# Performance work log

Hardware: AMD Instinct MI355X
Metric: run time of the kernel (lower is better)

The kernel has to match this reference:

```python
import jax, jax.numpy as jnp
import numpy as np

N_HEAD = 16

def setup_inputs() -> dict:
    key = jax.random.key(0)
    k1, k2, k3 = jax.random.split(key, 3)
    B, S, D = 4, 2048, 1024
    x = jax.random.normal(k1, (B, S, D), dtype=jnp.float32)
    w_attn = jax.random.normal(k2, (D, 3 * D), dtype=jnp.float32) * 0.02
    b_attn = jnp.zeros((3 * D,), dtype=jnp.float32)
    w_proj = jax.random.normal(k3, (D, D), dtype=jnp.float32) * 0.02
    b_proj = jnp.zeros((D,), dtype=jnp.float32)
    return {"x": x, "w_attn": w_attn, "b_attn": b_attn, "w_proj": w_proj, "b_proj": b_proj}

def reference(x, w_attn, b_attn, w_proj, b_proj):
    B, S, D = x.shape
    H = N_HEAD
    dh = D // H
    # c_attn (fan_in_fan_out Conv1D-style: y = x @ W + b)
    qkv = x @ w_attn + b_attn                      # [B,S,3D]
    q, k, v = jnp.split(qkv, 3, axis=-1)
    q = q.reshape(B, S, H, dh).transpose(0, 2, 1, 3)   # [B,H,S,dh]
    k = k.reshape(B, S, H, dh).transpose(0, 2, 3, 1)   # [B,H,dh,S]  (split_heads k=True)
    v = v.reshape(B, S, H, dh).transpose(0, 2, 1, 3)   # [B,H,S,dh]
    # scores = Q K^T, scaled by sqrt(d_head) since scale=True
    w = jnp.einsum('bhid,bhdj->bhij', q, k) / jnp.sqrt(jnp.asarray(dh, x.dtype))
    # causal mask blending exactly as original: w*b - 1e10*(1-b)
    b = jnp.tril(jnp.ones((S, S), dtype=x.dtype))[None, None]
    w = w * b - 1e10 * (1.0 - b)
    w = jax.nn.softmax(w, axis=-1)
    a = jnp.einsum('bhij,bhjd->bhid', w, v)        # [B,H,S,dh]
    a = a.transpose(0, 2, 1, 3).reshape(B, S, D)   # merge_heads
    out = a @ w_proj + b_proj                      # c_proj
    present = jnp.stack((k.transpose(0, 1, 3, 2), v))  # [2,B,H,S,dh]
    return out, present
```

## Files before the change

### kernel.cpp

```cpp
#include <hip/hip_runtime.h>
#include <stdint.h>

typedef unsigned short u16;
typedef __attribute__((ext_vector_type(8))) __bf16 bf16x8;
typedef __attribute__((ext_vector_type(4))) __bf16 bf16x4v;
typedef __attribute__((ext_vector_type(4))) float f32x4;
typedef __attribute__((ext_vector_type(4))) unsigned short u16x4;
typedef __attribute__((ext_vector_type(8))) unsigned short u16x8;

#define MFMA16(a,b,c) __builtin_amdgcn_mfma_f32_16x16x32_bf16(a,b,c,0,0,0)

static __device__ __forceinline__ float fexp2(float x){
#if __has_builtin(__builtin_amdgcn_exp2f)
  return __builtin_amdgcn_exp2f(x);
#else
  float r; asm("v_exp_f32 %0, %1" : "=v"(r) : "v"(x)); return r;
#endif
}

static __device__ __forceinline__ u16 f2b(float f){
  uint32_t u = __float_as_uint(f);
  u += 0x7fffu + ((u >> 16) & 1u);
  return (u16)(u >> 16);
}

static __device__ __forceinline__ void gload_lds16(const void* g, void* l){
  __builtin_amdgcn_global_load_lds(
      (__attribute__((address_space(1))) void*)(uintptr_t)g,
      (__attribute__((address_space(3))) void*)(uintptr_t)l,
      16, 0, 0);
}

__global__ __launch_bounds__(256) void cvt_bf16(const float* __restrict__ in,
                                                u16* __restrict__ out, int n){
  int i = (blockIdx.x * 256 + threadIdx.x) * 4;
  if (i >= n) return;
  float4 v = *(const float4*)(in + i);
  u16x4 o;
  o.x = f2b(v.x); o.y = f2b(v.y); o.z = f2b(v.z); o.w = f2b(v.w);
  *(u16x4*)(out + i) = o;
}

__global__ __launch_bounds__(256) void transpose_cvt(const float* __restrict__ in,
                                                     u16* __restrict__ out,
                                                     int K, int N){
  __shared__ float tile[32][33];
  const int nb = blockIdx.x * 32, kb = blockIdx.y * 32;
  const int tx = threadIdx.x, ty = threadIdx.y;
#pragma unroll
  for (int i = 0; i < 32; i += 8)
    tile[ty + i][tx] = in[(size_t)(kb + ty + i) * N + nb + tx];
  __syncthreads();
#pragma unroll
  for (int i = 0; i < 32; i += 8)
    out[(size_t)(nb + ty + i) * K + kb + tx] = f2b(tile[tx][ty + i]);
}

template<int MODE>
__global__ __launch_bounds__(256) void gemm_bf16(
    const u16* __restrict__ A, const u16* __restrict__ Bt,
    const float* __restrict__ bias, float* __restrict__ Cout,
    u16* __restrict__ q_bf, u16* __restrict__ k_bf, u16* __restrict__ vT_bf,
    int M, int N, int K)
{
  __shared__ u16 smem[16384];
  u16* As = smem;
  u16* Bs = smem + 8192;
  const int tid = threadIdx.x;
  const int w = tid >> 6, lane = tid & 63;
  const int l15 = lane & 15, lhi = lane >> 4;
  const int mBase = blockIdx.y * 128, nBase = blockIdx.x * 128;
  const int wr = w >> 1, wc = w & 1;

  f32x4 acc[4][4];
#pragma unroll
  for (int i = 0; i < 4; ++i)
#pragma unroll
    for (int j = 0; j < 4; ++j) acc[i][j] = f32x4{0.f, 0.f, 0.f, 0.f};

  const int nK = K >> 6;
  for (int kt = 0; kt < nK; ++kt){
    const int kb = kt << 6;
#pragma unroll
    for (int i = 0; i < 4; ++i){
      const int idx = i * 256 + tid;
      const int row = idx >> 3, c8 = idx & 7;
      gload_lds16(A  + (size_t)(mBase + row) * K + kb + c8 * 8,
                  As + (size_t)(i * 256 + w * 64) * 8);
      gload_lds16(Bt + (size_t)(nBase + row) * K + kb + c8 * 8,
                  Bs + (size_t)(i * 256 + w * 64) * 8);
    }
    __syncthreads();
#pragma unroll
    for (int kk = 0; kk < 2; ++kk){
      bf16x8 af[4], bb[4];
#pragma unroll
      for (int mi = 0; mi < 4; ++mi)
        af[mi] = *(const bf16x8*)&As[(wr * 64 + mi * 16 + l15) * 64 + kk * 32 + lhi * 8];
#pragma unroll
      for (int ni = 0; ni < 4; ++ni)
        bb[ni] = *(const bf16x8*)&Bs[(wc * 64 + ni * 16 + l15) * 64 + kk * 32 + lhi * 8];
#pragma unroll
      for (int mi = 0; mi < 4; ++mi)
#pragma unroll
        for (int ni = 0; ni < 4; ++ni)
          acc[mi][ni] = MFMA16(af[mi], bb[ni], acc[mi][ni]);
    }
    __syncthreads();
  }

  if (MODE == 0){
#pragma unroll
    for (int ni = 0; ni < 4; ++ni){
      const int col = nBase + wc * 64 + ni * 16 + l15;
      const float bv = bias[col];
#pragma unroll
      for (int mi = 0; mi < 4; ++mi)
#pragma unroll
        for (int r = 0; r < 4; ++r){
          const int row = mBase + wr * 64 + mi * 16 + lhi * 4 + r;
          Cout[(size_t)row * N + col] = acc[mi][ni][r] + bv;
        }
    }
    return;
  }

  const int sec = nBase >> 10;
  const int nn0 = nBase & 1023;
  const int bb  = mBase >> 11;
  const int s0  = mBase & 2047;

  if (sec == 2){
#pragma unroll
    for (int ni = 0; ni < 4; ++ni){
      const int c = wc * 64 + ni * 16 + l15;
      const int nn = nn0 + c;
      const int h = nn >> 6, d = nn & 63;
      const float bv = bias[nBase + c];
#pragma unroll
      for (int mi = 0; mi < 4; ++mi){
        const int sb = s0 + wr * 64 + mi * 16 + lhi * 4;
        u16x4 pk;
#pragma unroll
        for (int r = 0; r < 4; ++r){
          const float v = acc[mi][ni][r] + bv;
          pk[r] = f2b(v);
          Cout[16777216 + ((size_t)(bb * 16 + h) * 2048 + sb + r) * 64 + d] = v;
        }
        *(u16x4*)(vT_bf + ((size_t)(bb * 16 + h) * 64 + d) * 2048 + sb) = pk;
      }
    }
    return;
  }

  const float qscl = (sec == 0) ? 0.1803368801111204f : 1.0f;
#pragma unroll
  for (int ni = 0; ni < 4; ++ni){
    const int c = wc * 64 + ni * 16 + l15;
    const float bv = bias[nBase + c];
#pragma unroll
    for (int mi = 0; mi < 4; ++mi)
#pragma unroll
      for (int r = 0; r < 4; ++r){
        const int rl = wr * 64 + mi * 16 + lhi * 4 + r;
        const float v = (acc[mi][ni][r] + bv) * qscl;
        smem[rl * 128 + (c ^ ((rl & 7) << 3))] = f2b(v);
      }
  }
  if (sec == 1){
#pragma unroll
    for (int ni = 0; ni < 4; ++ni){
      const int c = wc * 64 + ni * 16 + l15;
      const int nn = nn0 + c;
      const int h = nn >> 6, d = nn & 63;
      const float bv = bias[nBase + c];
#pragma unroll
      for (int mi = 0; mi < 4; ++mi)
#pragma unroll
        for (int r = 0; r < 4; ++r){
          const int s = s0 + wr * 64 + mi * 16 + lhi * 4 + r;
          Cout[8388608 + ((size_t)(bb * 16 + h) * 2048 + s) * 64 + d] = acc[mi][ni][r] + bv;
        }
    }
  }
  __syncthreads();
  {
    const int rl = tid >> 1, hh = tid & 1;
    const int h = (nn0 >> 6) + hh;
    u16* dst = (sec == 0 ? q_bf : k_bf) + ((size_t)(bb * 16 + h) * 2048 + s0 + rl) * 64;
#pragma unroll
    for (int i = 0; i < 8; ++i){
      const int c0 = hh * 64 + i * 8;
      u16x8 vv = *(const u16x8*)&smem[rl * 128 + (c0 ^ ((rl & 7) << 3))];
      *(u16x8*)(dst + i * 8) = vv;
    }
  }
}

__global__ __launch_bounds__(256) void attn_kern(
    const u16* __restrict__ q_bf, const u16* __restrict__ k_bf,
    const u16* __restrict__ vT_bf, u16* __restrict__ a_bf)
{
  const int S = 2048;
  const int id = (int)blockIdx.x + 8 * (int)blockIdx.y;
  const int xcd = id & 7, j = id >> 3;
  const int bh = xcd + 8 * (j & 7);
  const int bx = j >> 3;

  const int tid = threadIdx.x, w = tid >> 6, lane = tid & 63;
  const int l15 = lane & 15, lhi = lane >> 4;
  const u16* qp = q_bf + (size_t)bh * S * 64;
  const char* kbytes = (const char*)(k_bf + (size_t)bh * S * 64);
  const char* vbytes = (const char*)(vT_bf + (size_t)bh * 64 * S);
  const int b = bh >> 4, h = bh & 15;

  __shared__ u16 Kbuf[2][64 * 64];
  __shared__ u16 Vbuf[2][64 * 64];
  __shared__ u16 P_all[4][32 * 64];
  char* Pc = (char*)&P_all[w][0];
  const int swz = (l15 & 7) << 4;

  const int srow = tid >> 3;
  const int sch  = (tid & 7) ^ (srow & 7);

  auto process = [&](f32x4 (&s)[4], float &m, float &l, f32x4 (&o)[4],
                     const bf16x8 (&vf)[8], int qr0g, bool domask, int jb, int gofs){
    if (domask){
      const int q = qr0g + l15;
#pragma unroll
      for (int nf = 0; nf < 4; ++nf)
#pragma unroll
        for (int r = 0; r < 4; ++r){
          const int kv = jb + nf * 16 + lhi * 4 + r;
          if (kv > q) s[nf][r] = -1e10f;
        }
    }
    float a0 = fmaxf(s[0][0], s[0][1]), a1 = fmaxf(s[0][2], s[0][3]);
    float a2 = fmaxf(s[1][0], s[1][1]), a3 = fmaxf(s[1][2], s[1][3]);
    float a4 = fmaxf(s[2][0], s[2][1]), a5 = fmaxf(s[2][2], s[2][3]);
    float a6 = fmaxf(s[3][0], s[3][1]), a7 = fmaxf(s[3][2], s[3][3]);
    float x = fmaxf(fmaxf(fmaxf(a0,a1), fmaxf(a2,a3)),
                    fmaxf(fmaxf(a4,a5), fmaxf(a6,a7)));
    x = fmaxf(x, __shfl_xor(x, 16));
    x = fmaxf(x, __shfl_xor(x, 32));
    if (__any(x - m > 8.0f)){
      const float mn = fmaxf(m, x);
      const float sc = fexp2(m - mn);
      m = mn;
      l *= sc;
      float scq[4];
#pragma unroll
      for (int r = 0; r < 4; ++r)
        scq[r] = __shfl(sc, (lane & 48) | (lhi * 4 + r));
#pragma unroll
      for (int df = 0; df < 4; ++df)
#pragma unroll
        for (int r = 0; r < 4; ++r) o[df][r] *= scq[r];
    }
    float p[16];
#pragma unroll
    for (int nf = 0; nf < 4; ++nf)
#pragma unroll
      for (int r = 0; r < 4; ++r) p[nf*4+r] = fexp2(s[nf][r] - m);
    float rs = (((p[0]+p[1])+(p[2]+p[3])) + ((p[4]+p[5])+(p[6]+p[7])))
             + (((p[8]+p[9])+(p[10]+p[11])) + ((p[12]+p[13])+(p[14]+p[15])));
    rs += __shfl_xor(rs, 16);
    rs += __shfl_xor(rs, 32);
    l += rs;
#pragma unroll
    for (int nf = 0; nf < 4; ++nf){
      bf16x4v pk;
#pragma unroll
      for (int r = 0; r < 4; ++r) pk[r] = (__bf16)p[nf*4+r];
      *(bf16x4v*)(Pc + gofs + ((l15 * 128 + nf * 32 + lhi * 8) ^ swz)) = pk;
    }
    __builtin_amdgcn_s_setprio(1);
#pragma unroll
    for (int kk = 0; kk < 2; ++kk){
      const bf16x8 pa = *(const bf16x8*)(Pc + gofs + ((l15 * 128 + kk * 64 + lhi * 16) ^ swz));
#pragma unroll
      for (int df = 0; df < 4; ++df)
        o[df] = MFMA16(pa, vf[kk*4+df], o[df]);
    }
    __builtin_amdgcn_s_setprio(0);
  };

  for (int half = 0; half < 2; ++half){
    const int qt = (half == 0) ? (15 - bx) : bx;
    const int qr0 = qt * 128 + w * 32;

    bf16x8 qf[2][2];
#pragma unroll
    for (int g = 0; g < 2; ++g){
      qf[g][0] = *(const bf16x8*)&qp[(qr0 + g * 16 + l15) * 64 + lhi * 8];
      qf[g][1] = *(const bf16x8*)&qp[(qr0 + g * 16 + l15) * 64 + 32 + lhi * 8];
    }

    f32x4 o[2][4];
#pragma unroll
    for (int g = 0; g < 2; ++g)
#pragma unroll
      for (int df = 0; df < 4; ++df) o[g][df] = f32x4{0.f,0.f,0.f,0.f};
    float m[2] = {-1e30f, -1e30f}, l[2] = {0.f, 0.f};

    const int nStage = 2 * qt + 2;
    const int nC = 2 * qt + 1 + (w >> 1);
    int cur = 0;

    gload_lds16(kbytes + (size_t)srow * 128 + sch * 16,        (char*)Kbuf[0] + w * 1024);
    gload_lds16(kbytes + (size_t)(srow + 32) * 128 + sch * 16, (char*)Kbuf[0] + 4096 + w * 1024);
    gload_lds16(vbytes + (size_t)srow * 4096 + sch * 16,        (char*)Vbuf[0] + w * 1024);
    gload_lds16(vbytes + (size_t)(srow + 32) * 4096 + sch * 16, (char*)Vbuf[0] + 4096 + w * 1024);
    __syncthreads();

    for (int it = 0; it < nStage; ++it){
      const int jb = it * 64;
      if (it + 1 < nStage){
        const char* kb2 = kbytes + (size_t)(jb + 64) * 128;
        const char* vb2 = vbytes + (size_t)(jb + 64) * 2;
        char* kd = (char*)Kbuf[cur ^ 1];
        char* vd = (char*)Vbuf[cur ^ 1];
        gload_lds16(kb2 + (size_t)srow * 128 + sch * 16,        kd + w * 1024);
        gload_lds16(kb2 + (size_t)(srow + 32) * 128 + sch * 16, kd + 4096 + w * 1024);
        gload_lds16(vb2 + (size_t)srow * 4096 + sch * 16,        vd + w * 1024);
        gload_lds16(vb2 + (size_t)(srow + 32) * 4096 + sch * 16, vd + 4096 + w * 1024);
      }
      if (it < nC){
        const char* Kc = (const char*)Kbuf[cur];
        const char* Vc = (const char*)Vbuf[cur];
        bf16x8 kf[8];
#pragma unroll
        for (int nf = 0; nf < 4; ++nf)
#pragma unroll
          for (int kk = 0; kk < 2; ++kk)
            kf[2*nf+kk] = *(const bf16x8*)(Kc + (((nf * 16 + l15) * 128 + kk * 64 + lhi * 16) ^ swz));
        f32x4 s[2][4];
        __builtin_amdgcn_s_setprio(1);
#pragma unroll
        for (int g = 0; g < 2; ++g)
#pragma unroll
          for (int nf = 0; nf < 4; ++nf){
            f32x4 z = {0.f, 0.f, 0.f, 0.f};
            z = MFMA16(kf[2*nf], qf[g][0], z);
            z = MFMA16(kf[2*nf+1], qf[g][1], z);
            s[g][nf] = z;
          }
        __builtin_amdgcn_s_setprio(0);
        bf16x8 vf[8];
#pragma unroll
        for (int kk = 0; kk < 2; ++kk)
#pragma unroll
          for (int df = 0; df < 4; ++df)
            vf[kk*4+df] = *(const bf16x8*)(Vc + (((df * 16 + l15) * 128 + kk * 64 + lhi * 16) ^ swz));
        const bool domask = (it == nC - 1);
        process(s[0], m[0], l[0], o[0], vf, qr0,      domask, jb, 0);
        process(s[1], m[1], l[1], o[1], vf, qr0 + 16, domask, jb, 2048);
      }
      __syncthreads();
      cur ^= 1;
    }

#pragma unroll
    for (int g = 0; g < 2; ++g){
      const float linv = 1.0f / l[g];
      float lr[4];
#pragma unroll
      for (int r = 0; r < 4; ++r)
        lr[r] = __shfl(linv, (lane & 48) | (lhi * 4 + r));
#pragma unroll
      for (int r = 0; r < 4; ++r){
        const int qrow = qr0 + g * 16 + lhi * 4 + r;
#pragma unroll
        for (int df = 0; df < 4; ++df)
          a_bf[((size_t)b * 2048 + qrow) * 1024 + h * 64 + df * 16 + l15] = f2b(o[g][df][r] * lr[r]);
      }
    }
  }
}

extern "C" void kernel_launch(void* const* d_in, const int* in_sizes, int n_in,
                              void* d_out, int out_size, void* d_ws, size_t ws_size,
                              hipStream_t stream)
{
  const float* x      = (const float*)d_in[0];
  const float* w_attn = (const float*)d_in[1];
  const float* b_attn = (const float*)d_in[2];
  const float* w_proj = (const float*)d_in[3];
  const float* b_proj = (const float*)d_in[4];
  float* out = (float*)d_out;
  char* ws = (char*)d_ws;
  const size_t MB = 1u << 20;
  u16* x_bf  = (u16*)(ws + 0);
  u16* wA_T  = (u16*)(ws + 16 * MB);
  u16* wP_T  = (u16*)(ws + 22 * MB);
  u16* q_bf  = (u16*)(ws + 24 * MB);
  u16* k_bf  = (u16*)(ws + 40 * MB);
  u16* vT_bf = (u16*)(ws + 56 * MB);
  u16* a_bf  = x_bf;

  cvt_bf16<<<dim3(8192), dim3(256), 0, stream>>>(x, x_bf, 4 * 2048 * 1024);
  transpose_cvt<<<dim3(96, 32), dim3(32, 8), 0, stream>>>(w_attn, wA_T, 1024, 3072);
  transpose_cvt<<<dim3(32, 32), dim3(32, 8), 0, stream>>>(w_proj, wP_T, 1024, 1024);
  gemm_bf16<1><<<dim3(24, 64), dim3(256), 0, stream>>>(
      x_bf, wA_T, b_attn, out, q_bf, k_bf, vT_bf, 8192, 3072, 1024);
  attn_kern<<<dim3(8, 64), dim3(256), 0, stream>>>(q_bf, k_bf, vT_bf, a_bf);
  gemm_bf16<0><<<dim3(8, 64), dim3(256), 0, stream>>>(
      a_bf, wP_T, b_proj, out, nullptr, nullptr, nullptr, 8192, 1024, 1024);
}
```

Measured before the change: 209.7 us.

## Replace QKV GEMM with 256x256 tiled, multi-buffered direct-to-LDS pipelined kernel

Splits the templated GEMM into a dedicated QKV kernel and a projection kernel. The QKV kernel uses 512 threads, 256x256 output tiles, K-step 32, and a 4-slot LDS ring filled by asynchronous global-to-LDS loads issued two stages ahead. It also uses swizzled LDS addressing and raises wave priority around the MFMA bursts. The aim is to hide memory latency and improve operand reuse in the largest GEMM. In exchange it needs 128KB of dynamic LDS per block and more accumulator registers, which caps occupancy.

```diff
diff --git a/kernel.cpp b/kernel.cpp
--- a/kernel.cpp
+++ b/kernel.cpp
@@ -56,16 +56,169 @@
     out[(size_t)(nb + ty + i) * K + kb + tx] = f2b(tile[tx][ty + i]);
 }
 
-template<int MODE>
-__global__ __launch_bounds__(256) void gemm_bf16(
+__global__ __launch_bounds__(512, 2) void gemm256_qkv(
     const u16* __restrict__ A, const u16* __restrict__ Bt,
     const float* __restrict__ bias, float* __restrict__ Cout,
-    u16* __restrict__ q_bf, u16* __restrict__ k_bf, u16* __restrict__ vT_bf,
+    u16* __restrict__ q_bf, u16* __restrict__ k_bf, u16* __restrict__ vT_bf)
+{
+  const int K = 1024;
+  const int nT = 32;
+  extern __shared__ u16 smem[];
+  const int tid = threadIdx.x;
+  const int w = tid >> 6, lane = tid & 63;
+  const int l15 = lane & 15, lhi = lane >> 4;
+  const int wr = w >> 2, wc = w & 3;
+  const int mBase = blockIdx.y * 256, nBase = blockIdx.x * 256;
+
+  const int srow = tid >> 2;
+  const int sch  = (tid & 3) ^ (srow & 3);
+  const u16* Ag = A  + (size_t)(mBase + srow) * K + sch * 8;
+  const u16* Bg = Bt + (size_t)(nBase + srow) * K + sch * 8;
+
+  f32x4 acc[8][4];
+#pragma unroll
+  for (int i = 0; i < 8; ++i)
+#pragma unroll
+    for (int j = 0; j < 4; ++j) acc[i][j] = f32x4{0.f, 0.f, 0.f, 0.f};
+
+  auto stageA = [&](int kt){
+    char* Ab = (char*)smem + (kt & 3) * 32768;
+    const int kb = kt << 5;
+    gload_lds16(Ag + kb,           Ab + tid * 16);
+    gload_lds16(Ag + 128 * K + kb, Ab + 8192 + tid * 16);
+  };
+  auto stageB = [&](int kt){
+    char* Bb = (char*)smem + (kt & 3) * 32768 + 16384;
+    const int kb = kt << 5;
+    gload_lds16(Bg + kb,           Bb + tid * 16);
+    gload_lds16(Bg + 128 * K + kb, Bb + 8192 + tid * 16);
+  };
+
+  stageA(0); stageB(0); stageA(1); stageB(1);
+
+  for (int kt = 0; kt < nT; ++kt){
+    if (kt == nT - 1) asm volatile("s_waitcnt vmcnt(0)" ::: "memory");
+    else              asm volatile("s_waitcnt vmcnt(4)" ::: "memory");
+    __builtin_amdgcn_s_barrier();
+    const char* Ab = (const char*)smem + (kt & 3) * 32768;
+    const char* Bb = Ab + 16384;
+
+    bf16x8 b0, b1, b2, b3, a0, a1, a2, a3;
+#define LDT(base, row) (*(const bf16x8*)((base) + ((row) << 6) + (((lhi ^ ((row) & 3))) << 4)))
+    {
+      const int br = wc * 64 + l15;
+      b0 = LDT(Bb, br); b1 = LDT(Bb, br + 16); b2 = LDT(Bb, br + 32); b3 = LDT(Bb, br + 48);
+      const int ar = wr * 128 + l15;
+      a0 = LDT(Ab, ar); a1 = LDT(Ab, ar + 16); a2 = LDT(Ab, ar + 32); a3 = LDT(Ab, ar + 48);
+    }
+    if (kt + 2 < nT) stageA(kt + 2);
+    __builtin_amdgcn_s_setprio(1);
+    acc[0][0] = MFMA16(a0, b0, acc[0][0]); acc[0][1] = MFMA16(a0, b1, acc[0][1]);
+    acc[0][2] = MFMA16(a0, b2, acc[0][2]); acc[0][3] = MFMA16(a0, b3, acc[0][3]);
+    acc[1][0] = MFMA16(a1, b0, acc[1][0]); acc[1][1] = MFMA16(a1, b1, acc[1][1]);
+    acc[1][2] = MFMA16(a1, b2, acc[1][2]); acc[1][3] = MFMA16(a1, b3, acc[1][3]);
+    acc[2][0] = MFMA16(a2, b0, acc[2][0]); acc[2][1] = MFMA16(a2, b1, acc[2][1]);
+    acc[2][2] = MFMA16(a2, b2, acc[2][2]); acc[2][3] = MFMA16(a2, b3, acc[2][3]);
+    acc[3][0] = MFMA16(a3, b0, acc[3][0]); acc[3][1] = MFMA16(a3, b1, acc[3][1]);
+    acc[3][2] = MFMA16(a3, b2, acc[3][2]); acc[3][3] = MFMA16(a3, b3, acc[3][3]);
+    __builtin_amdgcn_s_setprio(0);
+    {
+      const int ar = wr * 128 + 64 + l15;
+      a0 = LDT(Ab, ar); a1 = LDT(Ab, ar + 16); a2 = LDT(Ab, ar + 32); a3 = LDT(Ab, ar + 48);
+    }
+    if (kt + 2 < nT) stageB(kt + 2);
+    __builtin_amdgcn_s_setprio(1);
+    acc[4][0] = MFMA16(a0, b0, acc[4][0]); acc[4][1] = MFMA16(a0, b1, acc[4][1]);
+    acc[4][2] = MFMA16(a0, b2, acc[4][2]); acc[4][3] = MFMA16(a0, b3, acc[4][3]);
+    acc[5][0] = MFMA16(a1, b0, acc[5][0]); acc[5][1] = MFMA16(a1, b1, acc[5][1]);
+    acc[5][2] = MFMA16(a1, b2, acc[5][2]); acc[5][3] = MFMA16(a1, b3, acc[5][3]);
+    acc[6][0] = MFMA16(a2, b0, acc[6][0]); acc[6][1] = MFMA16(a2, b1, acc[6][1]);
+    acc[6][2] = MFMA16(a2, b2, acc[6][2]); acc[6][3] = MFMA16(a2, b3, acc[6][3]);
+    acc[7][0] = MFMA16(a3, b0, acc[7][0]); acc[7][1] = MFMA16(a3, b1, acc[7][1]);
+    acc[7][2] = MFMA16(a3, b2, acc[7][2]); acc[7][3] = MFMA16(a3, b3, acc[7][3]);
+    __builtin_amdgcn_s_setprio(0);
+#undef LDT
+  }
+  __syncthreads();
+
+  const int sec = nBase >> 10;
+  const int nn0 = nBase & 1023;
+  const int bb_ = mBase >> 11;
+  const int s0  = mBase & 2047;
+
+  if (sec == 2){
+#pragma unroll
+    for (int ni = 0; ni < 4; ++ni){
+      const int c = wc * 64 + ni * 16 + l15;
+      const int nn = nn0 + c;
+      const int h = nn >> 6, d = nn & 63;
+      const float bv = bias[nBase + c];
+#pragma unroll
+      for (int mi = 0; mi < 8; ++mi){
+        const int sb = s0 + wr * 128 + mi * 16 + lhi * 4;
+        u16x4 pk;
+#pragma unroll
+        for (int r = 0; r < 4; ++r){
+          const float v = acc[mi][ni][r] + bv;
+          pk[r] = f2b(v);
+          Cout[16777216 + ((size_t)(bb_ * 16 + h) * 2048 + sb + r) * 64 + d] = v;
+        }
+        *(u16x4*)(vT_bf + ((size_t)(bb_ * 16 + h) * 64 + d) * 2048 + sb) = pk;
+      }
+    }
+    return;
+  }
+
+  const float qscl = (sec == 0) ? 0.1803368801111204f : 1.0f;
+#pragma unroll
+  for (int ni = 0; ni < 4; ++ni){
+    const int c = wc * 64 + ni * 16 + l15;
+    const float bv = bias[nBase + c];
+#pragma unroll
+    for (int mi = 0; mi < 8; ++mi)
+#pragma unroll
+      for (int r = 0; r < 4; ++r){
+        const int rl = wr * 128 + mi * 16 + lhi * 4 + r;
+        smem[rl * 256 + (c ^ ((rl & 7) << 3))] = f2b((acc[mi][ni][r] + bv) * qscl);
+      }
+  }
+  if (sec == 1){
+#pragma unroll
+    for (int ni = 0; ni < 4; ++ni){
+      const int c = wc * 64 + ni * 16 + l15;
+      const int nn = nn0 + c;
+      const int h = nn >> 6, d = nn & 63;
+      const float bv = bias[nBase + c];
+#pragma unroll
+      for (int mi = 0; mi < 8; ++mi)
+#pragma unroll
+        for (int r = 0; r < 4; ++r){
+          const int s = s0 + wr * 128 + mi * 16 + lhi * 4 + r;
+          Cout[8388608 + ((size_t)(bb_ * 16 + h) * 2048 + s) * 64 + d] = acc[mi][ni][r] + bv;
+        }
+    }
+  }
+  __syncthreads();
+  {
+    const int row = tid >> 1, half = tid & 1;
+    u16* base = (sec == 0 ? q_bf : k_bf);
+#pragma unroll
+    for (int i = 0; i < 16; ++i){
+      const int c0 = half * 128 + i * 8;
+      const int h = (nn0 >> 6) + (c0 >> 6);
+      u16x8 vv = *(const u16x8*)&smem[row * 256 + (c0 ^ ((row & 7) << 3))];
+      *(u16x8*)(base + ((size_t)(bb_ * 16 + h) * 2048 + s0 + row) * 64 + (c0 & 63)) = vv;
+    }
+  }
+}
+
+__global__ __launch_bounds__(256) void gemm_proj(
+    const u16* __restrict__ A, const u16* __restrict__ Bt,
+    const float* __restrict__ bias, float* __restrict__ Cout,
     int M, int N, int K)
 {
-  __shared__ u16 smem[16384];
-  u16* As = smem;
-  u16* Bs = smem + 8192;
+  __shared__ u16 As[128 * 64];
+  __shared__ u16 Bs[128 * 64];
   const int tid = threadIdx.x;
   const int w = tid >> 6, lane = tid & 63;
   const int l15 = lane & 15, lhi = lane >> 4;
@@ -108,92 +261,17 @@
     }
     __syncthreads();
   }
-
-  if (MODE == 0){
-#pragma unroll
-    for (int ni = 0; ni < 4; ++ni){
-      const int col = nBase + wc * 64 + ni * 16 + l15;
-      const float bv = bias[col];
-#pragma unroll
-      for (int mi = 0; mi < 4; ++mi)
-#pragma unroll
-        for (int r = 0; r < 4; ++r){
-          const int row = mBase + wr * 64 + mi * 16 + lhi * 4 + r;
-          Cout[(size_t)row * N + col] = acc[mi][ni][r] + bv;
-        }
-    }
-    return;
-  }
-
-  const int sec = nBase >> 10;
-  const int nn0 = nBase & 1023;
-  const int bb  = mBase >> 11;
-  const int s0  = mBase & 2047;
-
-  if (sec == 2){
-#pragma unroll
-    for (int ni = 0; ni < 4; ++ni){
-      const int c = wc * 64 + ni * 16 + l15;
-      const int nn = nn0 + c;
-      const int h = nn >> 6, d = nn & 63;
-      const float bv = bias[nBase + c];
-#pragma unroll
-      for (int mi = 0; mi < 4; ++mi){
-        const int sb = s0 + wr * 64 + mi * 16 + lhi * 4;
-        u16x4 pk;
-#pragma unroll
-        for (int r = 0; r < 4; ++r){
-          const float v = acc[mi][ni][r] + bv;
-          pk[r] = f2b(v);
-          Cout[16777216 + ((size_t)(bb * 16 + h) * 2048 + sb + r) * 64 + d] = v;
-        }
-        *(u16x4*)(vT_bf + ((size_t)(bb * 16 + h) * 64 + d) * 2048 + sb) = pk;
-      }
-    }
-    return;
-  }
-
-  const float qscl = (sec == 0) ? 0.1803368801111204f : 1.0f;
 #pragma unroll
   for (int ni = 0; ni < 4; ++ni){
-    const int c = wc * 64 + ni * 16 + l15;
-    const float bv = bias[nBase + c];
+    const int col = nBase + wc * 64 + ni * 16 + l15;
+    const float bv = bias[col];
 #pragma unroll
     for (int mi = 0; mi < 4; ++mi)
 #pragma unroll
       for (int r = 0; r < 4; ++r){
-        const int rl = wr * 64 + mi * 16 + lhi * 4 + r;
-        const float v = (acc[mi][ni][r] + bv) * qscl;
-        smem[rl * 128 + (c ^ ((rl & 7) << 3))] = f2b(v);
-      }
-  }
-  if (sec == 1){
-#pragma unroll
-    for (int ni = 0; ni < 4; ++ni){
-      const int c = wc * 64 + ni * 16 + l15;
-      const int nn = nn0 + c;
-      const int h = nn >> 6, d = nn & 63;
-      const float bv = bias[nBase + c];
-#pragma unroll
-      for (int mi = 0; mi < 4; ++mi)
-#pragma unroll
-        for (int r = 0; r < 4; ++r){
-          const int s = s0 + wr * 64 + mi * 16 + lhi * 4 + r;
-          Cout[8388608 + ((size_t)(bb * 16 + h) * 2048 + s) * 64 + d] = acc[mi][ni][r] + bv;
-        }
-    }
-  }
-  __syncthreads();
-  {
-    const int rl = tid >> 1, hh = tid & 1;
-    const int h = (nn0 >> 6) + hh;
-    u16* dst = (sec == 0 ? q_bf : k_bf) + ((size_t)(bb * 16 + h) * 2048 + s0 + rl) * 64;
-#pragma unroll
-    for (int i = 0; i < 8; ++i){
-      const int c0 = hh * 64 + i * 8;
-      u16x8 vv = *(const u16x8*)&smem[rl * 128 + (c0 ^ ((rl & 7) << 3))];
-      *(u16x8*)(dst + i * 8) = vv;
-    }
+        const int row = mBase + wr * 64 + mi * 16 + lhi * 4 + r;
+        Cout[(size_t)row * N + col] = acc[mi][ni][r] + bv;
+      }
   }
 }
 
@@ -401,9 +479,9 @@
   cvt_bf16<<<dim3(8192), dim3(256), 0, stream>>>(x, x_bf, 4 * 2048 * 1024);
   transpose_cvt<<<dim3(96, 32), dim3(32, 8), 0, stream>>>(w_attn, wA_T, 1024, 3072);
   transpose_cvt<<<dim3(32, 32), dim3(32, 8), 0, stream>>>(w_proj, wP_T, 1024, 1024);
-  gemm_bf16<1><<<dim3(24, 64), dim3(256), 0, stream>>>(
-      x_bf, wA_T, b_attn, out, q_bf, k_bf, vT_bf, 8192, 3072, 1024);
+  gemm256_qkv<<<dim3(12, 32), dim3(512), 131072, stream>>>(
+      x_bf, wA_T, b_attn, out, q_bf, k_bf, vT_bf);
   attn_kern<<<dim3(8, 64), dim3(256), 0, stream>>>(q_bf, k_bf, vT_bf, a_bf);
-  gemm_bf16<0><<<dim3(8, 64), dim3(256), 0, stream>>>(
-      a_bf, wP_T, b_proj, out, nullptr, nullptr, nullptr, 8192, 1024, 1024);
-}
+  gemm_proj<<<dim3(8, 64), dim3(256), 0, stream>>>(
+      a_bf, wP_T, b_proj, out, 8192, 1024, 1024);
+}
```

Result: faster. 198.0 us (-5.6%).

## Replace GEMM with triple-buffered, 256x128-tile pipelined LDS kernel

Applied to the files above, without the earlier changes.

Both projection GEMMs now use a new 512-thread kernel with 256x128 output tiles and a K-step of 32. Direct-to-LDS loads are issued two stages ahead into a triple-buffered dynamic shared-memory ring, with manual vmcnt waits and a single barrier per step. LDS chunks are XOR-swizzled to cut bank conflicts, and MFMA sections run at raised wave priority. The aim is to hide global load latency behind MFMA work and drop the extra per-iteration barrier, at the cost of 72KB of LDS per block, which limits occupancy to two blocks per CU.

```diff
diff --git a/kernel.cpp b/kernel.cpp
--- a/kernel.cpp
+++ b/kernel.cpp
@@ -57,20 +57,25 @@
 }
 
 template<int MODE>
-__global__ __launch_bounds__(256) void gemm_bf16(
+__global__ __launch_bounds__(512, 2) void gemm_pipe(
     const u16* __restrict__ A, const u16* __restrict__ Bt,
     const float* __restrict__ bias, float* __restrict__ Cout,
     u16* __restrict__ q_bf, u16* __restrict__ k_bf, u16* __restrict__ vT_bf,
-    int M, int N, int K)
+    int N, int K)
 {
-  __shared__ u16 smem[16384];
-  u16* As = smem;
-  u16* Bs = smem + 8192;
+  extern __shared__ u16 smem[];
+  const int nT = K >> 5;
   const int tid = threadIdx.x;
   const int w = tid >> 6, lane = tid & 63;
   const int l15 = lane & 15, lhi = lane >> 4;
-  const int mBase = blockIdx.y * 128, nBase = blockIdx.x * 128;
   const int wr = w >> 1, wc = w & 1;
+  const int mBase = blockIdx.y * 256, nBase = blockIdx.x * 128;
+
+  const int r0 = tid >> 2;
+  const int ch = (tid & 3) ^ (r0 & 3);
+  const u16* Ag  = A  + (size_t)(mBase + r0) * K + ch * 8;
+  const u16* Ag2 = Ag + (size_t)128 * K;
+  const u16* Bg  = Bt + (size_t)(nBase + r0) * K + ch * 8;
 
   f32x4 acc[4][4];
 #pragma unroll
@@ -78,35 +83,42 @@
 #pragma unroll
     for (int j = 0; j < 4; ++j) acc[i][j] = f32x4{0.f, 0.f, 0.f, 0.f};
 
-  const int nK = K >> 6;
-  for (int kt = 0; kt < nK; ++kt){
-    const int kb = kt << 6;
-#pragma unroll
-    for (int i = 0; i < 4; ++i){
-      const int idx = i * 256 + tid;
-      const int row = idx >> 3, c8 = idx & 7;
-      gload_lds16(A  + (size_t)(mBase + row) * K + kb + c8 * 8,
-                  As + (size_t)(i * 256 + w * 64) * 8);
-      gload_lds16(Bt + (size_t)(nBase + row) * K + kb + c8 * 8,
-                  Bs + (size_t)(i * 256 + w * 64) * 8);
-    }
-    __syncthreads();
-#pragma unroll
-    for (int kk = 0; kk < 2; ++kk){
-      bf16x8 af[4], bb[4];
-#pragma unroll
-      for (int mi = 0; mi < 4; ++mi)
-        af[mi] = *(const bf16x8*)&As[(wr * 64 + mi * 16 + l15) * 64 + kk * 32 + lhi * 8];
-#pragma unroll
-      for (int ni = 0; ni < 4; ++ni)
-        bb[ni] = *(const bf16x8*)&Bs[(wc * 64 + ni * 16 + l15) * 64 + kk * 32 + lhi * 8];
-#pragma unroll
-      for (int mi = 0; mi < 4; ++mi)
-#pragma unroll
-        for (int ni = 0; ni < 4; ++ni)
-          acc[mi][ni] = MFMA16(af[mi], bb[ni], acc[mi][ni]);
-    }
-    __syncthreads();
+  auto stage = [&](int kt){
+    char* buf = (char*)smem + (kt % 3) * 24576;
+    const int kb = kt << 5;
+    gload_lds16(Ag  + kb, buf + tid * 16);
+    gload_lds16(Ag2 + kb, buf + 8192 + tid * 16);
+    gload_lds16(Bg  + kb, buf + 16384 + tid * 16);
+  };
+
+  stage(0); stage(1);
+
+  for (int kt = 0; kt < nT; ++kt){
+    if (kt == nT - 1) asm volatile("s_waitcnt vmcnt(0)" ::: "memory");
+    else              asm volatile("s_waitcnt vmcnt(3)" ::: "memory");
+    __builtin_amdgcn_s_barrier();
+    const char* Ab = (const char*)smem + (kt % 3) * 24576;
+    const char* Bb = Ab + 16384;
+#define LDT(base, row) (*(const bf16x8*)((base) + ((row) << 6) + (((lhi ^ ((row) & 3))) << 4)))
+    bf16x8 a0, a1, a2, a3, b0, b1, b2, b3;
+    {
+      const int ar = wr * 64 + l15;
+      a0 = LDT(Ab, ar); a1 = LDT(Ab, ar + 16); a2 = LDT(Ab, ar + 32); a3 = LDT(Ab, ar + 48);
+      const int br = wc * 64 + l15;
+      b0 = LDT(Bb, br); b1 = LDT(Bb, br + 16); b2 = LDT(Bb, br + 32); b3 = LDT(Bb, br + 48);
+    }
+#undef LDT
+    if (kt + 2 < nT) stage(kt + 2);
+    __builtin_amdgcn_s_setprio(1);
+    acc[0][0] = MFMA16(a0, b0, acc[0][0]); acc[0][1] = MFMA16(a0, b1, acc[0][1]);
+    acc[0][2] = MFMA16(a0, b2, acc[0][2]); acc[0][3] = MFMA16(a0, b3, acc[0][3]);
+    acc[1][0] = MFMA16(a1, b0, acc[1][0]); acc[1][1] = MFMA16(a1, b1, acc[1][1]);
+    acc[1][2] = MFMA16(a1, b2, acc[1][2]); acc[1][3] = MFMA16(a1, b3, acc[1][3]);
+    acc[2][0] = MFMA16(a2, b0, acc[2][0]); acc[2][1] = MFMA16(a2, b1, acc[2][1]);
+    acc[2][2] = MFMA16(a2, b2, acc[2][2]); acc[2][3] = MFMA16(a2, b3, acc[2][3]);
+    acc[3][0] = MFMA16(a3, b0, acc[3][0]); acc[3][1] = MFMA16(a3, b1, acc[3][1]);
+    acc[3][2] = MFMA16(a3, b2, acc[3][2]); acc[3][3] = MFMA16(a3, b3, acc[3][3]);
+    __builtin_amdgcn_s_setprio(0);
   }
 
   if (MODE == 0){
@@ -127,7 +139,7 @@
 
   const int sec = nBase >> 10;
   const int nn0 = nBase & 1023;
-  const int bb  = mBase >> 11;
+  const int bb_ = mBase >> 11;
   const int s0  = mBase & 2047;
 
   if (sec == 2){
@@ -145,14 +157,15 @@
         for (int r = 0; r < 4; ++r){
           const float v = acc[mi][ni][r] + bv;
           pk[r] = f2b(v);
-          Cout[16777216 + ((size_t)(bb * 16 + h) * 2048 + sb + r) * 64 + d] = v;
+          Cout[16777216 + ((size_t)(bb_ * 16 + h) * 2048 + sb + r) * 64 + d] = v;
         }
-        *(u16x4*)(vT_bf + ((size_t)(bb * 16 + h) * 64 + d) * 2048 + sb) = pk;
+        *(u16x4*)(vT_bf + ((size_t)(bb_ * 16 + h) * 64 + d) * 2048 + sb) = pk;
       }
     }
     return;
   }
 
+  __syncthreads();
   const float qscl = (sec == 0) ? 0.1803368801111204f : 1.0f;
 #pragma unroll
   for (int ni = 0; ni < 4; ++ni){
@@ -163,8 +176,7 @@
 #pragma unroll
       for (int r = 0; r < 4; ++r){
         const int rl = wr * 64 + mi * 16 + lhi * 4 + r;
-        const float v = (acc[mi][ni][r] + bv) * qscl;
-        smem[rl * 128 + (c ^ ((rl & 7) << 3))] = f2b(v);
+        smem[rl * 128 + (c ^ ((rl & 7) << 3))] = f2b((acc[mi][ni][r] + bv) * qscl);
       }
   }
   if (sec == 1){
@@ -179,20 +191,20 @@
 #pragma unroll
         for (int r = 0; r < 4; ++r){
           const int s = s0 + wr * 64 + mi * 16 + lhi * 4 + r;
-          Cout[8388608 + ((size_t)(bb * 16 + h) * 2048 + s) * 64 + d] = acc[mi][ni][r] + bv;
+          Cout[8388608 + ((size_t)(bb_ * 16 + h) * 2048 + s) * 64 + d] = acc[mi][ni][r] + bv;
         }
     }
   }
   __syncthreads();
   {
-    const int rl = tid >> 1, hh = tid & 1;
-    const int h = (nn0 >> 6) + hh;
-    u16* dst = (sec == 0 ? q_bf : k_bf) + ((size_t)(bb * 16 + h) * 2048 + s0 + rl) * 64;
+    const int row = tid >> 1, half = tid & 1;
+    u16* base = (sec == 0 ? q_bf : k_bf);
 #pragma unroll
     for (int i = 0; i < 8; ++i){
-      const int c0 = hh * 64 + i * 8;
-      u16x8 vv = *(const u16x8*)&smem[rl * 128 + (c0 ^ ((rl & 7) << 3))];
-      *(u16x8*)(dst + i * 8) = vv;
+      const int c0 = half * 64 + i * 8;
+      const int h = (nn0 >> 6) + (c0 >> 6);
+      u16x8 vv = *(const u16x8*)&smem[row * 128 + (c0 ^ ((row & 7) << 3))];
+      *(u16x8*)(base + ((size_t)(bb_ * 16 + h) * 2048 + s0 + row) * 64 + (c0 & 63)) = vv;
     }
   }
 }
@@ -401,9 +413,9 @@
   cvt_bf16<<<dim3(8192), dim3(256), 0, stream>>>(x, x_bf, 4 * 2048 * 1024);
   transpose_cvt<<<dim3(96, 32), dim3(32, 8), 0, stream>>>(w_attn, wA_T, 1024, 3072);
   transpose_cvt<<<dim3(32, 32), dim3(32, 8), 0, stream>>>(w_proj, wP_T, 1024, 1024);
-  gemm_bf16<1><<<dim3(24, 64), dim3(256), 0, stream>>>(
-      x_bf, wA_T, b_attn, out, q_bf, k_bf, vT_bf, 8192, 3072, 1024);
+  gemm_pipe<1><<<dim3(24, 32), dim3(512), 73728, stream>>>(
+      x_bf, wA_T, b_attn, out, q_bf, k_bf, vT_bf, 3072, 1024);
   attn_kern<<<dim3(8, 64), dim3(256), 0, stream>>>(q_bf, k_bf, vT_bf, a_bf);
-  gemm_bf16<0><<<dim3(8, 64), dim3(256), 0, stream>>>(
-      a_bf, wP_T, b_proj, out, nullptr, nullptr, nullptr, 8192, 1024, 1024);
-}
+  gemm_pipe<0><<<dim3(8, 32), dim3(512), 73728, stream>>>(
+      a_bf, wP_T, b_proj, out, nullptr, nullptr, nullptr, 1024, 1024);
+}
```

New measurement: 194.3 us. 7.3% less time.
